# Kernel tuning notes

Hardware: AMD Instinct MI355X
Metric: run time of the kernel (lower is better)

The kernel has to match this reference:

```python
import jax, jax.numpy as jnp
import numpy as np

N = 5
RANK = 4
IMW = IMH = 1024
S = IMW * IMH                 # flattened image size
M = N * (N + 3) // 2          # 20 factor matrices in the ParameterList


def setup_inputs() -> dict:
    key = jax.random.key(0)
    kz, kw, kb = jax.random.split(key, 3)
    z = jax.random.normal(kz, (S,), dtype=jnp.float32)
    # xavier_normal_ for an (s, rank) matrix: std = sqrt(2/(s+rank))
    std_w = float(np.sqrt(2.0 / (S + RANK)))
    W = jax.random.normal(kw, (M, S, RANK), dtype=jnp.float32) * std_w
    # b initialized as (s, 1) xavier: std = sqrt(2/(s+1))
    std_b = float(np.sqrt(2.0 / (S + 1)))
    b = jax.random.normal(kb, (S,), dtype=jnp.float32) * std_b
    return {"z": z, "W": W, "b": b}


def reference(z, W, b):
    # d[k-1, r] = dot(z, W[k][:, r]) for k = 1 .. N-2
    d = jnp.einsum('s,ksr->kr', z, W[1:N - 1])          # (N-2, rank)
    # Rsum_n uses prod_{k=1}^{n-1} d[k]; n=0 and n=1 contribute factor 1 each.
    coef = 2.0 + jnp.sum(jnp.cumprod(d, axis=0), axis=0)  # (rank,)
    # Nsum = sum_n sum_r W[0][:, r] * f_{n,r}  + b
    return W[0] @ coef + b
```

## Files before the change

kernel.cpp:

```cpp
#include <hip/hip_runtime.h>

static constexpr int S_TOT = 1024 * 1024;
static constexpr int RK = 4;
static constexpr int NK = 3;

__global__ __launch_bounds__(256) void dots_kernel(
    const float* __restrict__ z,
    const float* __restrict__ W,
    float* __restrict__ dsum) {
  float acc[NK][RK];
#pragma unroll
  for (int k = 0; k < NK; ++k)
#pragma unroll
    for (int r = 0; r < RK; ++r) acc[k][r] = 0.f;

  const int tid = blockIdx.x * blockDim.x + threadIdx.x;
  const int stride = gridDim.x * blockDim.x;
  for (int s = tid; s < S_TOT; s += stride) {
    const float zs = z[s];
#pragma unroll
    for (int k = 0; k < NK; ++k) {
      const float4 w = *reinterpret_cast<const float4*>(
          W + (size_t)(k + 1) * S_TOT * RK + (size_t)s * RK);
      acc[k][0] = fmaf(zs, w.x, acc[k][0]);
      acc[k][1] = fmaf(zs, w.y, acc[k][1]);
      acc[k][2] = fmaf(zs, w.z, acc[k][2]);
      acc[k][3] = fmaf(zs, w.w, acc[k][3]);
    }
  }

#pragma unroll
  for (int k = 0; k < NK; ++k)
#pragma unroll
    for (int r = 0; r < RK; ++r) {
      float v = acc[k][r];
#pragma unroll
      for (int off = 32; off > 0; off >>= 1) v += __shfl_xor(v, off, 64);
      acc[k][r] = v;
    }

  __shared__ float lds[4][NK * RK];
  const int wave = threadIdx.x >> 6;
  const int lane = threadIdx.x & 63;
  if (lane == 0) {
#pragma unroll
    for (int k = 0; k < NK; ++k)
#pragma unroll
      for (int r = 0; r < RK; ++r) lds[wave][k * RK + r] = acc[k][r];
  }
  __syncthreads();
  if (threadIdx.x < NK * RK) {
    float v = 0.f;
#pragma unroll
    for (int w = 0; w < 4; ++w) v += lds[w][threadIdx.x];
    atomicAdd(&dsum[threadIdx.x], v);
  }
}

__global__ __launch_bounds__(256) void out_kernel(
    const float* __restrict__ W0,
    const float* __restrict__ b,
    const float* __restrict__ dsum,
    float* __restrict__ out) {
  __shared__ float coef[RK];
  if (threadIdx.x < RK) {
    const int r = threadIdx.x;
    const float d0 = dsum[r];
    const float d1 = dsum[RK + r];
    const float d2 = dsum[2 * RK + r];
    const float c1 = d0;
    const float c2 = c1 * d1;
    const float c3 = c2 * d2;
    coef[r] = 2.f + c1 + c2 + c3;
  }
  __syncthreads();
  const float c0 = coef[0], c1 = coef[1], c2 = coef[2], c3 = coef[3];

  const int s = blockIdx.x * blockDim.x + threadIdx.x;
  if (s >= S_TOT) return;
  const float4 w = *reinterpret_cast<const float4*>(W0 + (size_t)s * RK);
  const float bs = b[s];
  out[s] = fmaf(w.x, c0, fmaf(w.y, c1, fmaf(w.z, c2, fmaf(w.w, c3, bs))));
}

extern "C" void kernel_launch(void* const* d_in, const int* in_sizes, int n_in,
                              void* d_out, int out_size, void* d_ws, size_t ws_size,
                              hipStream_t stream) {
  const float* z = (const float*)d_in[0];
  const float* W = (const float*)d_in[1];
  const float* b = (const float*)d_in[2];
  float* out = (float*)d_out;
  float* dsum = (float*)d_ws;

  hipMemsetAsync(dsum, 0, NK * RK * sizeof(float), stream);

  dots_kernel<<<2048, 256, 0, stream>>>(z, W, dsum);

  const int threads = 256;
  const int blocks = (S_TOT + threads - 1) / threads;
  out_kernel<<<blocks, threads, 0, stream>>>(W , b, dsum, out);
}
```

Baseline: 399.9 us.

## Replace atomic accumulation with per-block partials and a separate reduce kernel

The dot-product kernel now writes per-block partial sums to a workspace array instead of doing atomicAdd into a global accumulator. A new single-block kernel reduces the partials and computes the coefficients once, and the output kernel just reads them. This removes the memset launch and the atomic contention, and halves the grid of the dot-product kernel to 1024 blocks. The cost is an extra tiny kernel launch and possibly less latency hiding from the smaller grid.

```diff
diff --git a/kernel.cpp b/kernel.cpp
--- a/kernel.cpp
+++ b/kernel.cpp
@@ -3,11 +3,13 @@
 static constexpr int S_TOT = 1024 * 1024;
 static constexpr int RK = 4;
 static constexpr int NK = 3;
+static constexpr int NB1 = 1024;
+static constexpr int NCOMP = NK * RK;
 
-__global__ __launch_bounds__(256) void dots_kernel(
+__global__ __launch_bounds__(256) void dots_partial(
     const float* __restrict__ z,
     const float* __restrict__ W,
-    float* __restrict__ dsum) {
+    float* __restrict__ part) {
   float acc[NK][RK];
 #pragma unroll
   for (int k = 0; k < NK; ++k)
@@ -39,7 +41,7 @@
       acc[k][r] = v;
     }
 
-  __shared__ float lds[4][NK * RK];
+  __shared__ float lds[4][NCOMP];
   const int wave = threadIdx.x >> 6;
   const int lane = threadIdx.x & 63;
   if (lane == 0) {
@@ -49,30 +51,45 @@
       for (int r = 0; r < RK; ++r) lds[wave][k * RK + r] = acc[k][r];
   }
   __syncthreads();
-  if (threadIdx.x < NK * RK) {
+  if (threadIdx.x < NCOMP) {
     float v = 0.f;
 #pragma unroll
     for (int w = 0; w < 4; ++w) v += lds[w][threadIdx.x];
-    atomicAdd(&dsum[threadIdx.x], v);
+    part[threadIdx.x * NB1 + blockIdx.x] = v;
+  }
+}
+
+__global__ __launch_bounds__(64) void reduce_coef(
+    const float* __restrict__ part,
+    float* __restrict__ coef) {
+  const int lane = threadIdx.x;
+  float d[NCOMP];
+#pragma unroll
+  for (int c = 0; c < NCOMP; ++c) {
+    float v = 0.f;
+    for (int i = lane; i < NB1; i += 64) v += part[c * NB1 + i];
+#pragma unroll
+    for (int off = 32; off > 0; off >>= 1) v += __shfl_xor(v, off, 64);
+    d[c] = v;
+  }
+  if (lane < RK) {
+    const float d0 = d[lane];
+    const float d1 = d[RK + lane];
+    const float d2 = d[2 * RK + lane];
+    const float c1 = d0;
+    const float c2 = c1 * d1;
+    const float c3 = c2 * d2;
+    coef[lane] = 2.f + c1 + c2 + c3;
   }
 }
 
 __global__ __launch_bounds__(256) void out_kernel(
     const float* __restrict__ W0,
     const float* __restrict__ b,
-    const float* __restrict__ dsum,
+    const float* __restrict__ coefg,
     float* __restrict__ out) {
   __shared__ float coef[RK];
-  if (threadIdx.x < RK) {
-    const int r = threadIdx.x;
-    const float d0 = dsum[r];
-    const float d1 = dsum[RK + r];
-    const float d2 = dsum[2 * RK + r];
-    const float c1 = d0;
-    const float c2 = c1 * d1;
-    const float c3 = c2 * d2;
-    coef[r] = 2.f + c1 + c2 + c3;
-  }
+  if (threadIdx.x < RK) coef[threadIdx.x] = coefg[threadIdx.x];
   __syncthreads();
   const float c0 = coef[0], c1 = coef[1], c2 = coef[2], c3 = coef[3];
 
@@ -90,13 +107,14 @@
   const float* W = (const float*)d_in[1];
   const float* b = (const float*)d_in[2];
   float* out = (float*)d_out;
-  float* dsum = (float*)d_ws;
 
-  hipMemsetAsync(dsum, 0, NK * RK * sizeof(float), stream);
+  float* part = (float*)d_ws;
+  float* coef = part + NCOMP * NB1;
 
-  dots_kernel<<<2048, 256, 0, stream>>>(z, W, dsum);
+  dots_partial<<<NB1, 256, 0, stream>>>(z, W, part);
+  reduce_coef<<<1, 64, 0, stream>>>(part, coef);
 
   const int threads = 256;
   const int blocks = (S_TOT + threads - 1) / threads;
-  out_kernel<<<blocks, threads, 0, stream>>>(W , b, dsum, out);
+  out_kernel<<<blocks, threads, 0, stream>>>(W , b, coef, out);
 }
```

After: 433.2 us. 8.3% more time.
